# Performance work log

Measured on AMD Instinct MI355X. Metric: run time of the kernel, lower is better.

## Reference

```python
import jax, jax.numpy as jnp
import numpy as np
from jax import lax

D_MODEL = 1024
D_STATE = 16
D_CONV = 4
D_INNER = 2 * D_MODEL
BATCH = 2
SEQ = 1024


def setup_inputs() -> dict:
    key = jax.random.key(0)
    ks = jax.random.split(key, 8)
    std = 0.02
    return {
        "x": jax.random.normal(ks[0], (BATCH, SEQ, D_MODEL), jnp.float32),
        "in_proj_w": jax.random.normal(ks[1], (2 * D_INNER, D_MODEL), jnp.float32) * std,
        "conv_w": jax.random.normal(ks[2], (D_INNER, 1, D_CONV), jnp.float32) * 0.1,
        "x_proj_w": jax.random.normal(ks[3], (D_STATE + 1, D_INNER), jnp.float32) * std,
        "dt_w": jax.random.normal(ks[4], (D_INNER, 1), jnp.float32) * std,
        "dt_b": jnp.zeros((D_INNER,), jnp.float32),
        "A_param": jax.random.normal(ks[5], (D_INNER, D_STATE), jnp.float32) * std,
        "D_param": jnp.ones((D_INNER,), jnp.float32),
        "out_w": jax.random.normal(ks[6], (D_MODEL, D_INNER), jnp.float32) * std,
        "out_b": jnp.zeros((D_MODEL,), jnp.float32),
    }


def _silu(v):
    return v * jax.nn.sigmoid(v)


def _mamba_forward(x, in_proj_w, conv_w, x_proj_w, dt_w, dt_b, A_param, D_param, out_w, out_b):
    B, L, _ = x.shape
    # in_proj: [B,L,2*d_inner]
    xz = jnp.einsum('bld,ed->ble', x, in_proj_w)
    u, z = jnp.split(xz, 2, axis=-1)  # each [B,L,d_inner]
    # depthwise causal conv1d along time
    uc = u.transpose(0, 2, 1)  # [B,d_inner,L]
    uc = lax.conv_general_dilated(
        uc, conv_w, window_strides=(1,), padding=[(D_CONV - 1, D_CONV - 1)],
        dimension_numbers=('NCH', 'OIH', 'NCH'), feature_group_count=D_INNER,
    )[:, :, :L]
    u = _silu(uc.transpose(0, 2, 1))  # [B,L,d_inner]
    # x_proj -> (dt scalar, B coeffs)
    x_dbl = jnp.einsum('bld,ed->ble', u, x_proj_w)  # [B,L,d_state+1]
    dt_in = x_dbl[..., :1]                          # [B,L,1]
    Bmat = x_dbl[..., 1:]                           # [B,L,d_state]
    delta = jax.nn.softplus(dt_in * dt_w[:, 0] + dt_b)  # [B,L,d_inner]
    A = -jnp.exp(A_param)                            # [d_inner,d_state]

    # selective scan (time-major lax.scan)
    def step(h, inp):
        d_t, b_t = inp  # [B,d_inner], [B,d_state]
        h = jnp.exp(A * d_t[..., None]) * h + d_t[..., None] * b_t[:, None, :]
        y = jnp.einsum('bdn,bn->bd', h, b_t)
        return h, y

    h0 = jnp.zeros((B, D_INNER, D_STATE), x.dtype)
    _, ys = lax.scan(step, h0, (delta.transpose(1, 0, 2), Bmat.transpose(1, 0, 2)))
    y = ys.transpose(1, 0, 2) + u * D_param  # [B,L,d_inner]
    y = y * _silu(z)
    return jnp.einsum('bld,ed->ble', y, out_w) + out_b


def reference(x, in_proj_w, conv_w, x_proj_w, dt_w, dt_b, A_param, D_param, out_w, out_b):
    return _mamba_forward(x, in_proj_w, conv_w, x_proj_w, dt_w, dt_b, A_param, D_param, out_w, out_b)
```

## Files before the change

kernel.cpp:

```cpp
#include <hip/hip_runtime.h>
#include <stdint.h>
#include <stddef.h>

#define D_MODEL 1024
#define D_STATE 16
#define D_INNER 2048
#define BATCH   2
#define SEQ     1024
#define MROWS   (BATCH*SEQ)

#define NCH 16
#define TCH (SEQ/NCH)
#define NREC (BATCH*D_INNER*D_STATE)

#define XKS 8
#define XKC (D_INNER/XKS)

typedef __bf16 bf16x8 __attribute__((ext_vector_type(8)));
typedef float  f32x4  __attribute__((ext_vector_type(4)));

__device__ __forceinline__ unsigned short f2bf(float f) {
    unsigned int u = __float_as_uint(f);
    u += 0x7fffu + ((u >> 16) & 1u);
    return (unsigned short)(u >> 16);
}

__device__ __forceinline__ void gl_lds16(const unsigned short* g, unsigned short* l) {
    __builtin_amdgcn_global_load_lds(
        (const __attribute__((address_space(1))) unsigned int*)g,
        (__attribute__((address_space(3))) unsigned int*)l, 16, 0, 0);
}

__global__ void cvt_bf16_kernel(const float* __restrict__ src,
                                unsigned short* __restrict__ dst, int n) {
    int i = (blockIdx.x * blockDim.x + threadIdx.x) * 4;
    if (i < n) {
        float4 v = *(const float4*)(src + i);
        ushort4 o;
        o.x = f2bf(v.x); o.y = f2bf(v.y); o.z = f2bf(v.z); o.w = f2bf(v.w);
        *(ushort4*)(dst + i) = o;
    }
}

__global__ void cvt_xw_kernel(const float* __restrict__ xw,
                              unsigned short* __restrict__ wbp) {
    int id = blockIdx.x * 256 + threadIdx.x;
    wbp[id] = (id < 17 * D_INNER) ? f2bf(xw[id]) : (unsigned short)0;
}

template<bool BIAS>
__global__ void gemm_bf16_kernel(const unsigned short* __restrict__ A,
                                 const unsigned short* __restrict__ Bw,
                                 float* __restrict__ C,
                                 const float* __restrict__ bias,
                                 int M, int N, int K) {
    __shared__ __align__(16) unsigned short Al[128 * 32];
    __shared__ __align__(16) unsigned short Bl[128 * 32];

    const int tid  = threadIdx.x;
    const int lane = tid & 63;
    const int wid  = tid >> 6;
    const int wm   = wid >> 1;
    const int wn   = wid & 1;
    const int ln   = lane & 15;
    const int q    = lane >> 4;
    const int mblk = blockIdx.y * 128;
    const int nblk = blockIdx.x * 128;
    const int srow = lane >> 2;
    const int spart = lane & 3;

    f32x4 acc[4][4] = {};

    for (int k0 = 0; k0 < K; k0 += 32) {
        #pragma unroll
        for (int h = 0; h < 2; ++h) {
            int j = wid * 2 + h;
            int row = j * 16 + srow;
            gl_lds16(A  + (size_t)(mblk + row) * K + k0 + spart * 8, Al + j * 512);
            gl_lds16(Bw + (size_t)(nblk + row) * K + k0 + spart * 8, Bl + j * 512);
        }
        __syncthreads();

        bf16x8 af[4], bfr[4];
        #pragma unroll
        for (int mt = 0; mt < 4; ++mt)
            af[mt] = *(const bf16x8*)(Al + (wm * 64 + mt * 16 + ln) * 32 + q * 8);
        #pragma unroll
        for (int nt = 0; nt < 4; ++nt)
            bfr[nt] = *(const bf16x8*)(Bl + (wn * 64 + nt * 16 + ln) * 32 + q * 8);

        #pragma unroll
        for (int mt = 0; mt < 4; ++mt)
            #pragma unroll
            for (int nt = 0; nt < 4; ++nt)
                acc[mt][nt] = __builtin_amdgcn_mfma_f32_16x16x32_bf16(
                    af[mt], bfr[nt], acc[mt][nt], 0, 0, 0);
        __syncthreads();
    }

    #pragma unroll
    for (int mt = 0; mt < 4; ++mt) {
        #pragma unroll
        for (int nt = 0; nt < 4; ++nt) {
            int col = nblk + wn * 64 + nt * 16 + ln;
            float bv = BIAS ? bias[col] : 0.f;
            #pragma unroll
            for (int r = 0; r < 4; ++r) {
                int row = mblk + wm * 64 + mt * 16 + q * 4 + r;
                C[(size_t)row * N + col] = acc[mt][nt][r] + bv;
            }
        }
    }
}

__global__ void conv_silu_kernel(const float* __restrict__ xz,
                                 const float* __restrict__ conv_w,
                                 unsigned short* __restrict__ ub) {
    int idx = blockIdx.x * blockDim.x + threadIdx.x;
    int d = idx & (D_INNER - 1);
    int m = idx >> 11;
    int l = m & (SEQ - 1);
    const float* w = conv_w + d * 4;
    float s = 0.f;
    #pragma unroll
    for (int j = 0; j < 4; ++j) {
        if (l - j >= 0) s += w[3 - j] * xz[(size_t)(m - j) * 4096 + d];
    }
    float sig = 1.f / (1.f + __expf(-s));
    ub[idx] = f2bf(s * sig);
}

__global__ void xproj_mfma_kernel(const unsigned short* __restrict__ ub,
                                  const unsigned short* __restrict__ wbp,
                                  float* __restrict__ part) {
    __shared__ __align__(16) unsigned short Al[64 * 64];
    __shared__ __align__(16) unsigned short Bl[32 * 64];

    const int tid  = threadIdx.x;
    const int lane = tid & 63;
    const int wid  = tid >> 6;
    const int ln   = lane & 15;
    const int q    = lane >> 4;
    const int m0   = blockIdx.y * 64;
    const int ks   = blockIdx.x;
    const int srow = lane >> 3;
    const int spart = lane & 7;

    f32x4 acc[2] = {};

    for (int it = 0; it < 4; ++it) {
        int k0 = ks * XKC + it * 64;
        #pragma unroll
        for (int h = 0; h < 2; ++h) {
            int j = wid * 2 + h;
            int row = j * 8 + srow;
            gl_lds16(ub + (size_t)(m0 + row) * D_INNER + k0 + spart * 8, Al + j * 512);
        }
        {
            int row = wid * 8 + srow;
            gl_lds16(wbp + (size_t)row * D_INNER + k0 + spart * 8, Bl + wid * 512);
        }
        __syncthreads();

        bf16x8 af[2], bfr[2][2];
        #pragma unroll
        for (int kh = 0; kh < 2; ++kh) {
            af[kh] = *(const bf16x8*)(Al + (wid * 16 + ln) * 64 + kh * 32 + q * 8);
            bfr[0][kh] = *(const bf16x8*)(Bl + (0 * 16 + ln) * 64 + kh * 32 + q * 8);
            bfr[1][kh] = *(const bf16x8*)(Bl + (1 * 16 + ln) * 64 + kh * 32 + q * 8);
        }
        #pragma unroll
        for (int kh = 0; kh < 2; ++kh) {
            acc[0] = __builtin_amdgcn_mfma_f32_16x16x32_bf16(af[kh], bfr[0][kh], acc[0], 0, 0, 0);
            acc[1] = __builtin_amdgcn_mfma_f32_16x16x32_bf16(af[kh], bfr[1][kh], acc[1], 0, 0, 0);
        }
        __syncthreads();
    }

    #pragma unroll
    for (int nf = 0; nf < 2; ++nf) {
        #pragma unroll
        for (int r = 0; r < 4; ++r) {
            int m = m0 + wid * 16 + q * 4 + r;
            part[((size_t)ks * MROWS + m) * 32 + nf * 16 + ln] = acc[nf][r];
        }
    }
}

__global__ void xproj_reduce_kernel(const float* __restrict__ part,
                                    float* __restrict__ dti,
                                    float* __restrict__ Bm) {
    int id = blockIdx.x * 256 + threadIdx.x;
    int m = id >> 5, n = id & 31;
    float s = 0.f;
    #pragma unroll
    for (int ks = 0; ks < XKS; ++ks) s += part[(size_t)ks * MROWS * 32 + id];
    if (n == 0) dti[m] = s;
    else if (n < 17) Bm[(size_t)m * D_STATE + (n - 1)] = s;
}

__device__ __forceinline__ float softplus_f(float xv) {
    return fmaxf(xv, 0.f) + __logf(1.f + __expf(-fabsf(xv)));
}

__global__ void scanA_kernel(const float* __restrict__ dt_in,
                             const float* __restrict__ Bm,
                             const float* __restrict__ dt_w,
                             const float* __restrict__ dt_b,
                             const float* __restrict__ A_param,
                             float* __restrict__ Pg,
                             float* __restrict__ Sg) {
    __shared__ float sdt[TCH];
    __shared__ float sB[TCH * D_STATE];
    const int tid = threadIdx.x;
    const int b = blockIdx.z, c = blockIdx.y;
    const int d = blockIdx.x * 256 + tid;

    if (tid < TCH) sdt[tid] = dt_in[b * SEQ + c * TCH + tid];
    ((float4*)sB)[tid] = ((const float4*)(Bm + ((size_t)(b * SEQ + c * TCH)) * D_STATE))[tid];
    __syncthreads();

    const float dtw = dt_w[d], dtb = dt_b[d];
    float aA[D_STATE], h[D_STATE];
    #pragma unroll
    for (int n4 = 0; n4 < 4; ++n4) {
        float4 ap = ((const float4*)(A_param + (size_t)d * D_STATE))[n4];
        aA[n4*4+0] = -__expf(ap.x); aA[n4*4+1] = -__expf(ap.y);
        aA[n4*4+2] = -__expf(ap.z); aA[n4*4+3] = -__expf(ap.w);
    }
    #pragma unroll
    for (int n = 0; n < D_STATE; ++n) h[n] = 0.f;
    float tsum = 0.f;

    for (int t = 0; t < TCH; ++t) {
        float sp = softplus_f(sdt[t] * dtw + dtb);
        tsum += sp;
        #pragma unroll
        for (int n = 0; n < D_STATE; ++n) {
            float a = __expf(aA[n] * sp);
            h[n] = a * h[n] + sp * sB[t * D_STATE + n];
        }
    }

    size_t base = (size_t)c * NREC + ((size_t)(b * D_INNER + d)) * D_STATE;
    #pragma unroll
    for (int n4 = 0; n4 < 4; ++n4) {
        float4 pv, sv;
        pv.x = __expf(aA[n4*4+0] * tsum); pv.y = __expf(aA[n4*4+1] * tsum);
        pv.z = __expf(aA[n4*4+2] * tsum); pv.w = __expf(aA[n4*4+3] * tsum);
        sv.x = h[n4*4+0]; sv.y = h[n4*4+1]; sv.z = h[n4*4+2]; sv.w = h[n4*4+3];
        *(float4*)(Pg + base + n4 * 4) = pv;
        *(float4*)(Sg + base + n4 * 4) = sv;
    }
}

__global__ void scanB_kernel(const float* __restrict__ Pg,
                             const float* __restrict__ Sg,
                             float* __restrict__ Hin) {
    int idx = blockIdx.x * 256 + threadIdx.x;
    float h = 0.f;
    #pragma unroll
    for (int c = 0; c < NCH; ++c) {
        size_t o = (size_t)c * NREC + idx;
        Hin[o] = h;
        h = Pg[o] * h + Sg[o];
    }
}

__global__ void scanC_kernel(const float* __restrict__ dt_in,
                             const float* __restrict__ Bm,
                             const float* __restrict__ dt_w,
                             const float* __restrict__ dt_b,
                             const float* __restrict__ A_param,
                             const float* __restrict__ Hin,
                             float* __restrict__ ys) {
    __shared__ float sdt[TCH];
    __shared__ float sB[TCH * D_STATE];
    const int tid = threadIdx.x;
    const int b = blockIdx.z, c = blockIdx.y;
    const int d = blockIdx.x * 256 + tid;

    if (tid < TCH) sdt[tid] = dt_in[b * SEQ + c * TCH + tid];
    ((float4*)sB)[tid] = ((const float4*)(Bm + ((size_t)(b * SEQ + c * TCH)) * D_STATE))[tid];
    __syncthreads();

    const float dtw = dt_w[d], dtb = dt_b[d];
    float aA[D_STATE], h[D_STATE];
    #pragma unroll
    for (int n4 = 0; n4 < 4; ++n4) {
        float4 ap = ((const float4*)(A_param + (size_t)d * D_STATE))[n4];
        aA[n4*4+0] = -__expf(ap.x); aA[n4*4+1] = -__expf(ap.y);
        aA[n4*4+2] = -__expf(ap.z); aA[n4*4+3] = -__expf(ap.w);
    }
    size_t hbase = (size_t)c * NREC + ((size_t)(b * D_INNER + d)) * D_STATE;
    #pragma unroll
    for (int n4 = 0; n4 < 4; ++n4) {
        float4 hv = *(const float4*)(Hin + hbase + n4 * 4);
        h[n4*4+0] = hv.x; h[n4*4+1] = hv.y; h[n4*4+2] = hv.z; h[n4*4+3] = hv.w;
    }

    size_t ybase = ((size_t)b * SEQ + c * TCH) * D_INNER + d;
    for (int t = 0; t < TCH; ++t) {
        float sp = softplus_f(sdt[t] * dtw + dtb);
        float y0 = 0.f, y1 = 0.f, y2 = 0.f, y3 = 0.f;
        #pragma unroll
        for (int n4 = 0; n4 < 4; ++n4) {
            #pragma unroll
            for (int j = 0; j < 4; ++j) {
                int n = n4 * 4 + j;
                float Bv = sB[t * D_STATE + n];
                float a = __expf(aA[n] * sp);
                h[n] = a * h[n] + sp * Bv;
                float p = h[n] * Bv;
                if (n4 == 0) y0 += p; else if (n4 == 1) y1 += p;
                else if (n4 == 2) y2 += p; else y3 += p;
            }
        }
        ys[ybase + (size_t)t * D_INNER] = (y0 + y1) + (y2 + y3);
    }
}

__global__ void ypost_kernel(const float* __restrict__ ys,
                             const unsigned short* __restrict__ ub,
                             const float* __restrict__ xz,
                             const float* __restrict__ Dp,
                             unsigned short* __restrict__ ypb) {
    int idx = blockIdx.x * blockDim.x + threadIdx.x;
    int d = idx & (D_INNER - 1);
    int m = idx >> 11;
    float z  = xz[(size_t)m * 4096 + D_INNER + d];
    float sz = z / (1.f + __expf(-z));
    float uv = __uint_as_float((unsigned int)ub[idx] << 16);
    float yv = (ys[idx] + uv * Dp[d]) * sz;
    ypb[idx] = f2bf(yv);
}

extern "C" void kernel_launch(void* const* d_in, const int* in_sizes, int n_in,
                              void* d_out, int out_size, void* d_ws, size_t ws_size,
                              hipStream_t stream) {
    const float* x         = (const float*)d_in[0];
    const float* in_proj_w = (const float*)d_in[1];
    const float* conv_w    = (const float*)d_in[2];
    const float* x_proj_w  = (const float*)d_in[3];
    const float* dt_w      = (const float*)d_in[4];
    const float* dt_b      = (const float*)d_in[5];
    const float* A_param   = (const float*)d_in[6];
    const float* D_param   = (const float*)d_in[7];
    const float* out_w     = (const float*)d_in[8];
    const float* out_b     = (const float*)d_in[9];
    float* out = (float*)d_out;

    char* ws = (char*)d_ws;
    unsigned short* xb  = (unsigned short*)(ws);
    unsigned short* wbi = (unsigned short*)(ws + (4u  << 20));
    unsigned short* wbo = (unsigned short*)(ws + (12u << 20));
    float*          xz  = (float*)(ws + (16u << 20));
    unsigned short* ub  = (unsigned short*)(ws + (48u << 20));
    float*          dti = (float*)(ws + (56u << 20));
    float*          Bm  = (float*)(ws + (56u << 20) + (64u  << 10));
    unsigned short* wbp = (unsigned short*)(ws + (56u << 20) + (192u << 10));
    float*          xpt = (float*)(ws + (56u << 20) + (512u << 10));
    float*          ys  = (float*)(ws + (59u << 20));
    unsigned short* ypb = (unsigned short*)(ws + (75u << 20));
    float*          Pg  = (float*)(ws);
    float*          Sg  = (float*)(ws + (4u << 20));
    float*          Hin = (float*)(ws + (8u << 20));

    cvt_bf16_kernel<<<dim3(MROWS * D_MODEL / 1024), 256, 0, stream>>>(x, xb, MROWS * D_MODEL);
    cvt_bf16_kernel<<<dim3(2 * D_INNER * D_MODEL / 1024), 256, 0, stream>>>(in_proj_w, wbi, 2 * D_INNER * D_MODEL);
    cvt_bf16_kernel<<<dim3(D_MODEL * D_INNER / 1024), 256, 0, stream>>>(out_w, wbo, D_MODEL * D_INNER);
    cvt_xw_kernel<<<dim3(32 * D_INNER / 256), 256, 0, stream>>>(x_proj_w, wbp);

    gemm_bf16_kernel<false><<<dim3(4096 / 128, MROWS / 128), 256, 0, stream>>>(
        xb, wbi, xz, nullptr, MROWS, 2 * D_INNER, D_MODEL);

    conv_silu_kernel<<<dim3(MROWS * D_INNER / 256), 256, 0, stream>>>(xz, conv_w, ub);

    xproj_mfma_kernel<<<dim3(XKS, MROWS / 64), 256, 0, stream>>>(ub, wbp, xpt);
    xproj_reduce_kernel<<<dim3(MROWS * 32 / 256), 256, 0, stream>>>(xpt, dti, Bm);

    scanA_kernel<<<dim3(D_INNER / 256, NCH, BATCH), 256, 0, stream>>>(
        dti, Bm, dt_w, dt_b, A_param, Pg, Sg);
    scanB_kernel<<<dim3(NREC / 256), 256, 0, stream>>>(Pg, Sg, Hin);
    scanC_kernel<<<dim3(D_INNER / 256, NCH, BATCH), 256, 0, stream>>>(
        dti, Bm, dt_w, dt_b, A_param, Hin, ys);

    ypost_kernel<<<dim3(MROWS * D_INNER / 256), 256, 0, stream>>>(ys, ub, xz, D_param, ypb);

    gemm_bf16_kernel<true><<<dim3(1024 / 128, MROWS / 128), 256, 0, stream>>>(
        ypb, wbo, out, out_b, MROWS, D_MODEL, D_INNER);
}
```

Measured before the change: 254.5 us.

## Fuse conversions and y-postprocess into scan, double chunks, narrow out-proj tiles

```diff
diff --git a/kernel.cpp b/kernel.cpp
--- a/kernel.cpp
+++ b/kernel.cpp
@@ -9,7 +9,7 @@
 #define SEQ     1024
 #define MROWS   (BATCH*SEQ)
 
-#define NCH 16
+#define NCH 32
 #define TCH (SEQ/NCH)
 #define NREC (BATCH*D_INNER*D_STATE)
 
@@ -24,6 +24,9 @@
     u += 0x7fffu + ((u >> 16) & 1u);
     return (unsigned short)(u >> 16);
 }
+__device__ __forceinline__ float bf2f(unsigned short v) {
+    return __uint_as_float((unsigned int)v << 16);
+}
 
 __device__ __forceinline__ void gl_lds16(const unsigned short* g, unsigned short* l) {
     __builtin_amdgcn_global_load_lds(
@@ -31,31 +34,40 @@
         (__attribute__((address_space(3))) unsigned int*)l, 16, 0, 0);
 }
 
-__global__ void cvt_bf16_kernel(const float* __restrict__ src,
-                                unsigned short* __restrict__ dst, int n) {
-    int i = (blockIdx.x * blockDim.x + threadIdx.x) * 4;
-    if (i < n) {
+__global__ void cvt_all_kernel(const float* __restrict__ x,
+                               const float* __restrict__ w1,
+                               const float* __restrict__ w2,
+                               const float* __restrict__ xw,
+                               unsigned short* __restrict__ xb,
+                               unsigned short* __restrict__ wbi,
+                               unsigned short* __restrict__ wbo,
+                               unsigned short* __restrict__ wbp) {
+    int blk = blockIdx.x, tid = threadIdx.x;
+    if (blk < 8192) {
+        const float* src; unsigned short* dst; int i;
+        if (blk < 2048)      { src = x;  dst = xb;  i = blk * 1024 + tid * 4; }
+        else if (blk < 6144) { src = w1; dst = wbi; i = (blk - 2048) * 1024 + tid * 4; }
+        else                 { src = w2; dst = wbo; i = (blk - 6144) * 1024 + tid * 4; }
         float4 v = *(const float4*)(src + i);
         ushort4 o;
         o.x = f2bf(v.x); o.y = f2bf(v.y); o.z = f2bf(v.z); o.w = f2bf(v.w);
         *(ushort4*)(dst + i) = o;
-    }
-}
-
-__global__ void cvt_xw_kernel(const float* __restrict__ xw,
-                              unsigned short* __restrict__ wbp) {
-    int id = blockIdx.x * 256 + threadIdx.x;
-    wbp[id] = (id < 17 * D_INNER) ? f2bf(xw[id]) : (unsigned short)0;
-}
-
-template<bool BIAS>
+    } else {
+        int id = (blk - 8192) * 256 + tid;
+        wbp[id] = (id < 17 * D_INNER) ? f2bf(xw[id]) : (unsigned short)0;
+    }
+}
+
+template<int NT, bool BIAS>
 __global__ void gemm_bf16_kernel(const unsigned short* __restrict__ A,
                                  const unsigned short* __restrict__ Bw,
                                  float* __restrict__ C,
                                  const float* __restrict__ bias,
                                  int M, int N, int K) {
+    constexpr int NTW  = NT / 32;
+    constexpr int BCHW = NT / 64;
     __shared__ __align__(16) unsigned short Al[128 * 32];
-    __shared__ __align__(16) unsigned short Bl[128 * 32];
+    __shared__ __align__(16) unsigned short Bl[NT * 32];
 
     const int tid  = threadIdx.x;
     const int lane = tid & 63;
@@ -65,34 +77,39 @@
     const int ln   = lane & 15;
     const int q    = lane >> 4;
     const int mblk = blockIdx.y * 128;
-    const int nblk = blockIdx.x * 128;
+    const int nblk = blockIdx.x * NT;
     const int srow = lane >> 2;
     const int spart = lane & 3;
 
-    f32x4 acc[4][4] = {};
+    f32x4 acc[4][NTW] = {};
 
     for (int k0 = 0; k0 < K; k0 += 32) {
         #pragma unroll
         for (int h = 0; h < 2; ++h) {
             int j = wid * 2 + h;
             int row = j * 16 + srow;
-            gl_lds16(A  + (size_t)(mblk + row) * K + k0 + spart * 8, Al + j * 512);
+            gl_lds16(A + (size_t)(mblk + row) * K + k0 + spart * 8, Al + j * 512);
+        }
+        #pragma unroll
+        for (int h = 0; h < BCHW; ++h) {
+            int j = wid * BCHW + h;
+            int row = j * 16 + srow;
             gl_lds16(Bw + (size_t)(nblk + row) * K + k0 + spart * 8, Bl + j * 512);
         }
         __syncthreads();
 
-        bf16x8 af[4], bfr[4];
+        bf16x8 af[4], bfr[NTW];
         #pragma unroll
         for (int mt = 0; mt < 4; ++mt)
             af[mt] = *(const bf16x8*)(Al + (wm * 64 + mt * 16 + ln) * 32 + q * 8);
         #pragma unroll
-        for (int nt = 0; nt < 4; ++nt)
-            bfr[nt] = *(const bf16x8*)(Bl + (wn * 64 + nt * 16 + ln) * 32 + q * 8);
+        for (int nt = 0; nt < NTW; ++nt)
+            bfr[nt] = *(const bf16x8*)(Bl + (wn * (NT/2) + nt * 16 + ln) * 32 + q * 8);
 
         #pragma unroll
         for (int mt = 0; mt < 4; ++mt)
             #pragma unroll
-            for (int nt = 0; nt < 4; ++nt)
+            for (int nt = 0; nt < NTW; ++nt)
                 acc[mt][nt] = __builtin_amdgcn_mfma_f32_16x16x32_bf16(
                     af[mt], bfr[nt], acc[mt][nt], 0, 0, 0);
         __syncthreads();
@@ -101,8 +118,8 @@
     #pragma unroll
     for (int mt = 0; mt < 4; ++mt) {
         #pragma unroll
-        for (int nt = 0; nt < 4; ++nt) {
-            int col = nblk + wn * 64 + nt * 16 + ln;
+        for (int nt = 0; nt < NTW; ++nt) {
+            int col = nblk + wn * (NT/2) + nt * 16 + ln;
             float bv = BIAS ? bias[col] : 0.f;
             #pragma unroll
             for (int r = 0; r < 4; ++r) {
@@ -217,7 +234,8 @@
     const int d = blockIdx.x * 256 + tid;
 
     if (tid < TCH) sdt[tid] = dt_in[b * SEQ + c * TCH + tid];
-    ((float4*)sB)[tid] = ((const float4*)(Bm + ((size_t)(b * SEQ + c * TCH)) * D_STATE))[tid];
+    if (tid < TCH * D_STATE / 4)
+        ((float4*)sB)[tid] = ((const float4*)(Bm + ((size_t)(b * SEQ + c * TCH)) * D_STATE))[tid];
     __syncthreads();
 
     const float dtw = dt_w[d], dtb = dt_b[d];
@@ -273,7 +291,10 @@
                              const float* __restrict__ dt_b,
                              const float* __restrict__ A_param,
                              const float* __restrict__ Hin,
-                             float* __restrict__ ys) {
+                             const unsigned short* __restrict__ ub,
+                             const float* __restrict__ xz,
+                             const float* __restrict__ Dp,
+                             unsigned short* __restrict__ ypb) {
     __shared__ float sdt[TCH];
     __shared__ float sB[TCH * D_STATE];
     const int tid = threadIdx.x;
@@ -281,10 +302,12 @@
     const int d = blockIdx.x * 256 + tid;
 
     if (tid < TCH) sdt[tid] = dt_in[b * SEQ + c * TCH + tid];
-    ((float4*)sB)[tid] = ((const float4*)(Bm + ((size_t)(b * SEQ + c * TCH)) * D_STATE))[tid];
+    if (tid < TCH * D_STATE / 4)
+        ((float4*)sB)[tid] = ((const float4*)(Bm + ((size_t)(b * SEQ + c * TCH)) * D_STATE))[tid];
     __syncthreads();
 
     const float dtw = dt_w[d], dtb = dt_b[d];
+    const float Dv = Dp[d];
     float aA[D_STATE], h[D_STATE];
     #pragma unroll
     for (int n4 = 0; n4 < 4; ++n4) {
@@ -299,7 +322,7 @@
         h[n4*4+0] = hv.x; h[n4*4+1] = hv.y; h[n4*4+2] = hv.z; h[n4*4+3] = hv.w;
     }
 
-    size_t ybase = ((size_t)b * SEQ + c * TCH) * D_INNER + d;
+    const size_t mrow0 = (size_t)b * SEQ + c * TCH;
     for (int t = 0; t < TCH; ++t) {
         float sp = softplus_f(sdt[t] * dtw + dtb);
         float y0 = 0.f, y1 = 0.f, y2 = 0.f, y3 = 0.f;
@@ -316,23 +339,13 @@
                 else if (n4 == 2) y2 += p; else y3 += p;
             }
         }
-        ys[ybase + (size_t)t * D_INNER] = (y0 + y1) + (y2 + y3);
-    }
-}
-
-__global__ void ypost_kernel(const float* __restrict__ ys,
-                             const unsigned short* __restrict__ ub,
-                             const float* __restrict__ xz,
-                             const float* __restrict__ Dp,
-                             unsigned short* __restrict__ ypb) {
-    int idx = blockIdx.x * blockDim.x + threadIdx.x;
-    int d = idx & (D_INNER - 1);
-    int m = idx >> 11;
-    float z  = xz[(size_t)m * 4096 + D_INNER + d];
-    float sz = z / (1.f + __expf(-z));
-    float uv = __uint_as_float((unsigned int)ub[idx] << 16);
-    float yv = (ys[idx] + uv * Dp[d]) * sz;
-    ypb[idx] = f2bf(yv);
+        float y = (y0 + y1) + (y2 + y3);
+        size_t m = mrow0 + t;
+        float z  = xz[m * 4096 + D_INNER + d];
+        float sz = z / (1.f + __expf(-z));
+        float uv = bf2f(ub[m * D_INNER + d]);
+        ypb[m * D_INNER + d] = f2bf((y + uv * Dv) * sz);
+    }
 }
 
 extern "C" void kernel_launch(void* const* d_in, const int* in_sizes, int n_in,
@@ -360,18 +373,15 @@
     float*          Bm  = (float*)(ws + (56u << 20) + (64u  << 10));
     unsigned short* wbp = (unsigned short*)(ws + (56u << 20) + (192u << 10));
     float*          xpt = (float*)(ws + (56u << 20) + (512u << 10));
-    float*          ys  = (float*)(ws + (59u << 20));
-    unsigned short* ypb = (unsigned short*)(ws + (75u << 20));
-    float*          Pg  = (float*)(ws);
-    float*          Sg  = (float*)(ws + (4u << 20));
-    float*          Hin = (float*)(ws + (8u << 20));
-
-    cvt_bf16_kernel<<<dim3(MROWS * D_MODEL / 1024), 256, 0, stream>>>(x, xb, MROWS * D_MODEL);
-    cvt_bf16_kernel<<<dim3(2 * D_INNER * D_MODEL / 1024), 256, 0, stream>>>(in_proj_w, wbi, 2 * D_INNER * D_MODEL);
-    cvt_bf16_kernel<<<dim3(D_MODEL * D_INNER / 1024), 256, 0, stream>>>(out_w, wbo, D_MODEL * D_INNER);
-    cvt_xw_kernel<<<dim3(32 * D_INNER / 256), 256, 0, stream>>>(x_proj_w, wbp);
-
-    gemm_bf16_kernel<false><<<dim3(4096 / 128, MROWS / 128), 256, 0, stream>>>(
+    float*          Pg  = (float*)(ws + (59u << 20));
+    float*          Sg  = (float*)(ws + (67u << 20));
+    float*          Hin = (float*)(ws + (75u << 20));
+    unsigned short* ypb = (unsigned short*)(ws + (83u << 20));
+
+    cvt_all_kernel<<<dim3(8448), 256, 0, stream>>>(
+        x, in_proj_w, out_w, x_proj_w, xb, wbi, wbo, wbp);
+
+    gemm_bf16_kernel<128, false><<<dim3(4096 / 128, MROWS / 128), 256, 0, stream>>>(
         xb, wbi, xz, nullptr, MROWS, 2 * D_INNER, D_MODEL);
 
     conv_silu_kernel<<<dim3(MROWS * D_INNER / 256), 256, 0, stream>>>(xz, conv_w, ub);
@@ -383,10 +393,8 @@
         dti, Bm, dt_w, dt_b, A_param, Pg, Sg);
     scanB_kernel<<<dim3(NREC / 256), 256, 0, stream>>>(Pg, Sg, Hin);
     scanC_kernel<<<dim3(D_INNER / 256, NCH, BATCH), 256, 0, stream>>>(
-        dti, Bm, dt_w, dt_b, A_param, Hin, ys);
-
-    ypost_kernel<<<dim3(MROWS * D_INNER / 256), 256, 0, stream>>>(ys, ub, xz, D_param, ypb);
-
-    gemm_bf16_kernel<true><<<dim3(1024 / 128, MROWS / 128), 256, 0, stream>>>(
+        dti, Bm, dt_w, dt_b, A_param, Hin, ub, xz, D_param, ypb);
+
+    gemm_bf16_kernel<64, true><<<dim3(1024 / 64, MROWS / 128), 256, 0, stream>>>(
         ypb, wbo, out, out_b, MROWS, D_MODEL, D_INNER);
 }
```

Measured after the change: 238.8 us. 1.07x faster.
